# Kernel optimization log

Hardware: AMD Instinct MI355X
Metric: run time of the kernel (lower is better)

The kernel has to match this reference:

```python
import jax, jax.numpy as jnp
import numpy as np

B, S, D = 4, 2048, 1024  # batch, seq_len, d_emb (even for Givens pairs)


def givens_rotate(r, x):
    """Apply 2x2 Givens block rotations defined by r [D] to x [..., D]."""
    g = r.reshape(-1, 2)
    g = g / jnp.linalg.norm(g, axis=-1, keepdims=True)  # normalize (cos, sin) pairs
    xp = x.reshape(x.shape[:-1] + (x.shape[-1] // 2, 2))
    c, s = g[:, 0], g[:, 1]
    y0 = c * xp[..., 0] - s * xp[..., 1]
    y1 = c * xp[..., 1] + s * xp[..., 0]
    return jnp.stack([y0, y1], axis=-1).reshape(x.shape)


def setup_inputs() -> dict:
    key = jax.random.key(0)
    k1, k2 = jax.random.split(key, 2)
    Q = jax.random.normal(k1, (B, S, D), dtype=jnp.float32)
    # QKV_rotation.weight ~ U(-1, 1) per original init (before the identity overwrite)
    rot_w = jax.random.uniform(k2, (3, D), dtype=jnp.float32, minval=-1.0, maxval=1.0)
    scale = jnp.array([np.sqrt(D)], dtype=jnp.float32)
    bias = jnp.zeros((), dtype=jnp.float32)
    return {"Q": Q, "rot_w": rot_w, "scale": scale, "bias": bias}


def reference(Q, rot_w, scale, bias):
    # Givens-rotation 'projections' for q/k/v
    q = givens_rotate(rot_w[0], Q)
    k = givens_rotate(rot_w[1], Q)
    v = givens_rotate(rot_w[2], Q)
    # prepend zero time coordinate -> points on the Lorentz model ambient space
    zeros = jnp.zeros(Q.shape[:-1] + (1,), Q.dtype)
    q = jnp.concatenate([zeros, q], axis=-1)[:, None]  # [B,1,S,D+1]
    k = jnp.concatenate([zeros, k], axis=-1)[:, None]
    v = jnp.concatenate([zeros, v], axis=-1)[:, None]
    # Lorentz signature (-, +, +, ...)
    sgn = jnp.concatenate([-jnp.ones((1,), Q.dtype), jnp.ones((q.shape[-1] - 1,), Q.dtype)])
    # cinner(q, k): time-negated inner product -> scores [B,1,S,S]
    cin = jnp.einsum('bhqd,bhkd->bhqk', q * sgn, k)
    attn = jax.nn.softmax((2.0 + 2.0 * cin) / scale + bias, axis=-1)
    # Lorentz mid-point: weighted sum normalized by sqrt(|<m,m>_L|)
    ave = jnp.einsum('bhqk,bhkd->bhqd', attn, v)
    inner = jnp.sum(ave * ave * sgn, axis=-1, keepdims=True)
    denom = jnp.sqrt(jnp.clip(jnp.abs(inner), 1e-8, None))
    out = (ave / denom)[:, 0]  # [B,S,D+1]
    return out[..., 1:]  # drop time coordinate -> [B,S,D]
```

## Files before the change

### kernel.cpp

```cpp
#include <hip/hip_runtime.h>

typedef _Float16 h16;
typedef _Float16 half8 __attribute__((ext_vector_type(8)));
typedef _Float16 half4v __attribute__((ext_vector_type(4)));
typedef float floatx4 __attribute__((ext_vector_type(4)));

static constexpr int Bb_ = 4, S_ = 2048, D_ = 1024;

static __device__ __forceinline__ void gl_lds16(const void* g, void* l) {
  __builtin_amdgcn_global_load_lds(
      (const __attribute__((address_space(1))) unsigned int*)g,
      (__attribute__((address_space(3))) unsigned int*)l, 16, 0, 0);
}

__global__ __launch_bounds__(256) void k_prep_t(const float* __restrict__ Q,
                                                const float* __restrict__ rot,
                                                h16* __restrict__ Qh,
                                                h16* __restrict__ Kh,
                                                h16* __restrict__ VhT) {
  __shared__ __align__(16) h16 tile[64][64];
  int d0 = blockIdx.x * 64, s0 = blockIdx.y * 64, b = blockIdx.z;
  int t = threadIdx.x;
  const float* Qb = Q + ((size_t)b * S_ + s0) * D_ + d0;
  h16* Qhb = Qh + ((size_t)b * S_ + s0) * D_ + d0;
  h16* Khb = Kh + ((size_t)b * S_ + s0) * D_ + d0;
#pragma unroll
  for (int i = 0; i < 4; ++i) {
    int c = t + 256 * i;
    int row = c >> 4;
    int col = (c & 15) * 4;
    float4 q = *(const float4*)&Qb[(size_t)row * D_ + col];
    int dg = (d0 + col) >> 2;
    float4 r0 = ((const float4*)rot)[dg];
    float4 r1 = ((const float4*)rot)[D_ / 4 + dg];
    float4 r2 = ((const float4*)rot)[2 * D_ / 4 + dg];
    float inq0 = rsqrtf(r0.x * r0.x + r0.y * r0.y);
    float ink0 = rsqrtf(r1.x * r1.x + r1.y * r1.y);
    float cc0 = (r0.x * r1.x + r0.y * r1.y) * inq0 * ink0;
    float ss0 = (r0.x * r1.y - r0.y * r1.x) * inq0 * ink0;
    float y0 = cc0 * q.x - ss0 * q.y;
    float y1 = cc0 * q.y + ss0 * q.x;
    float inq1 = rsqrtf(r0.z * r0.z + r0.w * r0.w);
    float ink1 = rsqrtf(r1.z * r1.z + r1.w * r1.w);
    float cc1 = (r0.z * r1.z + r0.w * r1.w) * inq1 * ink1;
    float ss1 = (r0.z * r1.w - r0.w * r1.z) * inq1 * ink1;
    float y2 = cc1 * q.z - ss1 * q.w;
    float y3 = cc1 * q.w + ss1 * q.z;
    float inv0 = rsqrtf(r2.x * r2.x + r2.y * r2.y);
    float cv0 = r2.x * inv0, sv0 = r2.y * inv0;
    float v0 = cv0 * q.x - sv0 * q.y;
    float v1 = cv0 * q.y + sv0 * q.x;
    float inv1 = rsqrtf(r2.z * r2.z + r2.w * r2.w);
    float cv1 = r2.z * inv1, sv1 = r2.w * inv1;
    float v2 = cv1 * q.z - sv1 * q.w;
    float v3 = cv1 * q.w + sv1 * q.z;
    half4v kh = {(h16)y0, (h16)y1, (h16)y2, (h16)y3};
    half4v qh = {(h16)q.x, (h16)q.y, (h16)q.z, (h16)q.w};
    half4v vh = {(h16)v0, (h16)v1, (h16)v2, (h16)v3};
    *(half4v*)&Qhb[(size_t)row * D_ + col] = qh;
    *(half4v*)&Khb[(size_t)row * D_ + col] = kh;
    int pcol = col ^ ((row >> 3) << 3);
    *(half4v*)&tile[row][pcol] = vh;
  }
  __syncthreads();
  h16* dst = VhT + ((size_t)b * D_ + d0) * S_ + s0;
#pragma unroll
  for (int i = 0; i < 2; ++i) {
    int c = t + 256 * i;
    int drow = c >> 3;
    int sc = (c & 7) * 8;
    int xr = sc;
    half8 v;
#pragma unroll
    for (int j = 0; j < 8; ++j) v[j] = tile[sc + j][drow ^ xr];
    *(half8*)&dst[(size_t)drow * S_ + sc] = v;
  }
}

template <bool OUT16>
__global__ __launch_bounds__(256) void k_gemm_bt(
    const char* __restrict__ A, int a_pitch, unsigned long long a_batch,
    const char* __restrict__ Bt, int b_pitch, unsigned long long b_batch,
    void* __restrict__ C, int c_pitch, unsigned long long c_batch, int Kdim) {
  __shared__ __align__(16) h16 As[2][128 * 32];
  __shared__ __align__(16) h16 Bs[2][128 * 32];
  const int t = threadIdx.x;
  const int lane = t & 63;
  const int w = t >> 6;
  const int wm = (w >> 1) * 64;
  const int wn = (w & 1) * 64;

  const int id = blockIdx.x + gridDim.x * (blockIdx.y + 16 * blockIdx.z);
  const int xcd = id & 7;
  const int s = id >> 3;
  int tm, tn, tz;
  if constexpr (OUT16) {
    tz = s >> 5;
    int tt = s & 31;
    tm = (xcd >> 1) * 4 + (tt >> 3);
    tn = (xcd & 1) * 8 + (tt & 7);
  } else {
    tz = s >> 4;
    int tt = s & 15;
    tm = (xcd >> 1) * 4 + (tt >> 2);
    tn = (xcd & 1) * 4 + (tt & 3);
  }

  const char* Ab = A + (unsigned long long)tz * a_batch +
                   (unsigned long long)tm * 128ull * (unsigned long long)a_pitch;
  const char* Bbp = Bt + (unsigned long long)tz * b_batch +
                    (unsigned long long)tn * 128ull * (unsigned long long)b_pitch;
  const int o0 = t * 16;
  const int o1 = o0 + 4096;
  const int ar0 = o0 >> 6, ar1 = o1 >> 6;
  const int ac0 = ((((o0 >> 4) & 3) ^ ((ar0 >> 1) & 3)) << 4);
  const int ac1 = ((((o1 >> 4) & 3) ^ ((ar1 >> 1) & 3)) << 4);
  const int mrow = lane & 15;
  const int kc = lane >> 4;
  const int koff = ((kc ^ ((mrow >> 1) & 3)) << 3);

  floatx4 acc[4][4];
#pragma unroll
  for (int i = 0; i < 4; ++i)
#pragma unroll
    for (int j = 0; j < 4; ++j) acc[i][j] = (floatx4){0.f, 0.f, 0.f, 0.f};

  for (int kt = 0; kt < Kdim; kt += 64) {
    const int kb = kt * 2;
#pragma unroll
    for (int h = 0; h < 2; ++h) {
      const int hb = kb + h * 64;
      gl_lds16(Ab + (unsigned long long)ar0 * a_pitch + hb + ac0, (char*)As[h] + o0);
      gl_lds16(Ab + (unsigned long long)ar1 * a_pitch + hb + ac1, (char*)As[h] + o1);
      gl_lds16(Bbp + (unsigned long long)ar0 * b_pitch + hb + ac0, (char*)Bs[h] + o0);
      gl_lds16(Bbp + (unsigned long long)ar1 * b_pitch + hb + ac1, (char*)Bs[h] + o1);
    }
    __syncthreads();
#pragma unroll
    for (int h = 0; h < 2; ++h) {
      half8 a[4], b[4];
#pragma unroll
      for (int i = 0; i < 4; ++i)
        a[i] = *(const half8*)&As[h][(wm + i * 16 + mrow) * 32 + koff];
#pragma unroll
      for (int i = 0; i < 4; ++i)
        b[i] = *(const half8*)&Bs[h][(wn + i * 16 + mrow) * 32 + koff];
#pragma unroll
      for (int i = 0; i < 4; ++i)
#pragma unroll
        for (int j = 0; j < 4; ++j)
          acc[i][j] = __builtin_amdgcn_mfma_f32_16x16x32_f16(a[i], b[j], acc[i][j], 0, 0, 0);
    }
    __syncthreads();
  }

  const int m0 = tm * 128 + wm;
  const int n0 = tn * 128 + wn;
  const int col = lane & 15;
  const int rquad = (lane >> 4) * 4;
  if constexpr (OUT16) {
    h16* Cb = (h16*)C + (unsigned long long)tz * c_batch;
#pragma unroll
    for (int i = 0; i < 4; ++i)
#pragma unroll
      for (int j = 0; j < 4; ++j)
#pragma unroll
        for (int r = 0; r < 4; ++r)
          Cb[(unsigned long long)(m0 + i * 16 + rquad + r) * c_pitch + (n0 + j * 16 + col)] =
              (h16)acc[i][j][r];
  } else {
    float* Cb = (float*)C + (unsigned long long)tz * c_batch;
#pragma unroll
    for (int i = 0; i < 4; ++i)
#pragma unroll
      for (int j = 0; j < 4; ++j)
#pragma unroll
        for (int r = 0; r < 4; ++r)
          Cb[(unsigned long long)(m0 + i * 16 + rquad + r) * c_pitch + (n0 + j * 16 + col)] =
              acc[i][j][r];
  }
}

__global__ __launch_bounds__(256) void k_softmax(h16* __restrict__ Sl,
                                                 const float* __restrict__ scale_p) {
  int wv = threadIdx.x >> 6, ln = threadIdx.x & 63;
  int row = blockIdx.x * 4 + wv;
  h16* base = Sl + (size_t)row * S_;
  half8 c[4];
#pragma unroll
  for (int r = 0; r < 4; ++r) c[r] = ((const half8*)base)[ln + 64 * r];
  float m = -1e30f;
#pragma unroll
  for (int r = 0; r < 4; ++r)
#pragma unroll
    for (int j = 0; j < 8; ++j) m = fmaxf(m, (float)c[r][j]);
#pragma unroll
  for (int off = 32; off; off >>= 1) m = fmaxf(m, __shfl_xor(m, off));
  float alpha = 2.0f / scale_p[0];
#pragma unroll
  for (int r = 0; r < 4; ++r) {
    half8 pv;
#pragma unroll
    for (int j = 0; j < 8; ++j) pv[j] = (h16)__expf(((float)c[r][j] - m) * alpha);
    ((half8*)base)[ln + 64 * r] = pv;
  }
}

__global__ __launch_bounds__(256) void k_epilogue(float* __restrict__ O) {
  int wv = threadIdx.x >> 6, ln = threadIdx.x & 63;
  int row = blockIdx.x * 4 + wv;
  float* base = O + (size_t)row * D_;
  float4 u[4];
#pragma unroll
  for (int r = 0; r < 4; ++r) u[r] = ((const float4*)base)[ln + 64 * r];
  float ss = 0.f;
#pragma unroll
  for (int r = 0; r < 4; ++r)
    ss += u[r].x * u[r].x + u[r].y * u[r].y + u[r].z * u[r].z + u[r].w * u[r].w;
#pragma unroll
  for (int off = 32; off; off >>= 1) ss += __shfl_xor(ss, off);
  float f = rsqrtf(fmaxf(ss, 1e-30f));
#pragma unroll
  for (int r = 0; r < 4; ++r) {
    float4 o;
    o.x = u[r].x * f;
    o.y = u[r].y * f;
    o.z = u[r].z * f;
    o.w = u[r].w * f;
    ((float4*)base)[ln + 64 * r] = o;
  }
}

extern "C" void kernel_launch(void* const* d_in, const int* in_sizes, int n_in,
                              void* d_out, int out_size, void* d_ws, size_t ws_size,
                              hipStream_t stream) {
  const float* Q = (const float*)d_in[0];
  const float* rot = (const float*)d_in[1];
  const float* scale = (const float*)d_in[2];
  float* O = (float*)d_out;
  char* ws = (char*)d_ws;
  const size_t MB = 1024ull * 1024ull;
  h16* Qh = (h16*)(ws);
  h16* Kh = (h16*)(ws + 16 * MB);
  h16* VhT = (h16*)(ws + 32 * MB);
  h16* Sl = (h16*)(ws + 48 * MB);

  k_prep_t<<<dim3(D_ / 64, S_ / 64, Bb_), 256, 0, stream>>>(Q, rot, Qh, Kh, VhT);
  k_gemm_bt<true><<<dim3(S_ / 128, S_ / 128, Bb_), 256, 0, stream>>>(
      (const char*)Qh, D_ * 2, (unsigned long long)S_ * D_ * 2,
      (const char*)Kh, D_ * 2, (unsigned long long)S_ * D_ * 2,
      (void*)Sl, S_, (unsigned long long)S_ * S_, D_);
  k_softmax<<<dim3(Bb_ * S_ / 4), 256, 0, stream>>>(Sl, scale);
  k_gemm_bt<false><<<dim3(D_ / 128, S_ / 128, Bb_), 256, 0, stream>>>(
      (const char*)Sl, S_ * 2, (unsigned long long)S_ * S_ * 2,
      (const char*)VhT, S_ * 2, (unsigned long long)D_ * S_ * 2,
      (void*)O, D_, (unsigned long long)S_ * D_, S_);
  k_epilogue<<<dim3(Bb_ * S_ / 4), 256, 0, stream>>>(O);
}
```

Before: 209.2 us.

## Replace 128x128 GEMM with 8-wave 256-row tiled, prefetch-pipelined GEMM

Replaces the 4-wave 128x128 tile GEMM with an 8-wave, 512-thread kernel using 256x256 (QK^T) or 256x128 (PV) tiles. It double-buffers LDS, issues global-to-LDS loads for future k-tiles between MFMA quads, and uses explicit vmcnt waits, barriers and s_setprio to overlap loads with compute. Block-to-tile mapping is changed to group tiles per XCD. The larger per-thread accumulator footprint may lower occupancy, and the fine-grained barrier schedule is fragile.

```diff
diff --git a/kernel.cpp b/kernel.cpp
--- a/kernel.cpp
+++ b/kernel.cpp
@@ -77,108 +77,185 @@
   }
 }
 
-template <bool OUT16>
-__global__ __launch_bounds__(256) void k_gemm_bt(
+#define G_FENCE asm volatile("" ::: "memory")
+#define G_BAR                     \
+  do {                            \
+    G_FENCE;                      \
+    __builtin_amdgcn_s_barrier(); \
+    G_FENCE;                      \
+  } while (0)
+
+template <int NF, bool OUT16>
+__global__ __launch_bounds__(512) void k_gemm8(
     const char* __restrict__ A, int a_pitch, unsigned long long a_batch,
     const char* __restrict__ Bt, int b_pitch, unsigned long long b_batch,
     void* __restrict__ C, int c_pitch, unsigned long long c_batch, int Kdim) {
-  __shared__ __align__(16) h16 As[2][128 * 32];
-  __shared__ __align__(16) h16 Bs[2][128 * 32];
+  constexpr int BNR = NF * 64;
+  constexpr int JQ = NF / 2;
+  __shared__ __align__(16) h16 As[2][2][256 * 32];
+  __shared__ __align__(16) h16 Bs[2][2][BNR * 32];
   const int t = threadIdx.x;
   const int lane = t & 63;
   const int w = t >> 6;
-  const int wm = (w >> 1) * 64;
-  const int wn = (w & 1) * 64;
-
-  const int id = blockIdx.x + gridDim.x * (blockIdx.y + 16 * blockIdx.z);
-  const int xcd = id & 7;
-  const int s = id >> 3;
-  int tm, tn, tz;
-  if constexpr (OUT16) {
-    tz = s >> 5;
-    int tt = s & 31;
-    tm = (xcd >> 1) * 4 + (tt >> 3);
-    tn = (xcd & 1) * 8 + (tt & 7);
-  } else {
-    tz = s >> 4;
-    int tt = s & 15;
-    tm = (xcd >> 1) * 4 + (tt >> 2);
-    tn = (xcd & 1) * 4 + (tt & 3);
-  }
-
+  const int wm = (w >> 2) * 128;
+  const int wn = (w & 3) * (NF * 16);
+  const int id = blockIdx.x + 8 * (blockIdx.y + 8 * blockIdx.z);
+  const int L = (id & 7) * 32 + (id >> 3);
+  const int tm = L & 7, tn = (L >> 3) & 7, tz = L >> 6;
   const char* Ab = A + (unsigned long long)tz * a_batch +
-                   (unsigned long long)tm * 128ull * (unsigned long long)a_pitch;
-  const char* Bbp = Bt + (unsigned long long)tz * b_batch +
-                    (unsigned long long)tn * 128ull * (unsigned long long)b_pitch;
-  const int o0 = t * 16;
-  const int o1 = o0 + 4096;
-  const int ar0 = o0 >> 6, ar1 = o1 >> 6;
-  const int ac0 = ((((o0 >> 4) & 3) ^ ((ar0 >> 1) & 3)) << 4);
-  const int ac1 = ((((o1 >> 4) & 3) ^ ((ar1 >> 1) & 3)) << 4);
-  const int mrow = lane & 15;
-  const int kc = lane >> 4;
-  const int koff = ((kc ^ ((mrow >> 1) & 3)) << 3);
-
-  floatx4 acc[4][4];
-#pragma unroll
-  for (int i = 0; i < 4; ++i)
-#pragma unroll
-    for (int j = 0; j < 4; ++j) acc[i][j] = (floatx4){0.f, 0.f, 0.f, 0.f};
-
-  for (int kt = 0; kt < Kdim; kt += 64) {
-    const int kb = kt * 2;
-#pragma unroll
-    for (int h = 0; h < 2; ++h) {
-      const int hb = kb + h * 64;
-      gl_lds16(Ab + (unsigned long long)ar0 * a_pitch + hb + ac0, (char*)As[h] + o0);
-      gl_lds16(Ab + (unsigned long long)ar1 * a_pitch + hb + ac1, (char*)As[h] + o1);
-      gl_lds16(Bbp + (unsigned long long)ar0 * b_pitch + hb + ac0, (char*)Bs[h] + o0);
-      gl_lds16(Bbp + (unsigned long long)ar1 * b_pitch + hb + ac1, (char*)Bs[h] + o1);
-    }
-    __syncthreads();
-#pragma unroll
-    for (int h = 0; h < 2; ++h) {
-      half8 a[4], b[4];
-#pragma unroll
-      for (int i = 0; i < 4; ++i)
-        a[i] = *(const half8*)&As[h][(wm + i * 16 + mrow) * 32 + koff];
-#pragma unroll
-      for (int i = 0; i < 4; ++i)
-        b[i] = *(const half8*)&Bs[h][(wn + i * 16 + mrow) * 32 + koff];
-#pragma unroll
-      for (int i = 0; i < 4; ++i)
-#pragma unroll
-        for (int j = 0; j < 4; ++j)
-          acc[i][j] = __builtin_amdgcn_mfma_f32_16x16x32_f16(a[i], b[j], acc[i][j], 0, 0, 0);
-    }
-    __syncthreads();
-  }
-
-  const int m0 = tm * 128 + wm;
-  const int n0 = tn * 128 + wn;
-  const int col = lane & 15;
-  const int rquad = (lane >> 4) * 4;
+                   (unsigned long long)(tm * 256) * (unsigned long long)a_pitch;
+  const char* Bb = Bt + (unsigned long long)tz * b_batch +
+                   (unsigned long long)(tn * BNR) * (unsigned long long)b_pitch;
+  const int srow = t >> 2;
+  const int scol = ((t & 3) ^ ((t >> 3) & 3)) << 4;
+  const int lds_o = t * 16;
+  const int mrow = lane & 15, kc = lane >> 4;
+  const int koff = (kc ^ ((mrow >> 1) & 3)) << 3;
+  const int NT = Kdim >> 6;
+
+#define SG_A(bf, kt, hm)                                                      \
+  do {                                                                        \
+    const char* sp_ = Ab +                                                    \
+                      (unsigned long long)(srow + (hm) * 128) * a_pitch +     \
+                      (kt) * 128 + scol;                                      \
+    gl_lds16(sp_, (char*)&As[bf][0][(hm) * 128 * 32] + lds_o);                \
+    gl_lds16(sp_ + 64, (char*)&As[bf][1][(hm) * 128 * 32] + lds_o);           \
+  } while (0)
+#define SG_B(bf, kt, hm)                                                      \
+  do {                                                                        \
+    const char* sp_ = Bb +                                                    \
+                      (unsigned long long)(srow + (hm) * 128) * b_pitch +     \
+                      (kt) * 128 + scol;                                      \
+    gl_lds16(sp_, (char*)&Bs[bf][0][(hm) * 128 * 32] + lds_o);                \
+    gl_lds16(sp_ + 64, (char*)&Bs[bf][1][(hm) * 128 * 32] + lds_o);           \
+  } while (0)
+
+  half8 a[4][2], b[2][JQ][2];
+  floatx4 acc[8][NF];
+#pragma unroll
+  for (int i = 0; i < 8; ++i)
+#pragma unroll
+    for (int j = 0; j < NF; ++j) acc[i][j] = (floatx4){0.f, 0.f, 0.f, 0.f};
+
+#define LDA_(bf, mh)                                                           \
+  do {                                                                         \
+    _Pragma("unroll") for (int i_ = 0; i_ < 4; ++i_) {                         \
+      a[i_][0] = *(const half8*)&As[bf][0]                                     \
+                     [(wm + ((mh) * 4 + i_) * 16 + mrow) * 32 + koff];         \
+      a[i_][1] = *(const half8*)&As[bf][1]                                     \
+                     [(wm + ((mh) * 4 + i_) * 16 + mrow) * 32 + koff];         \
+    }                                                                          \
+  } while (0)
+#define LDB_(bf, nh)                                                           \
+  do {                                                                         \
+    _Pragma("unroll") for (int j_ = 0; j_ < JQ; ++j_) {                        \
+      b[nh][j_][0] = *(const half8*)&Bs[bf][0]                                 \
+                         [(wn + ((nh) * JQ + j_) * 16 + mrow) * 32 + koff];    \
+      b[nh][j_][1] = *(const half8*)&Bs[bf][1]                                 \
+                         [(wn + ((nh) * JQ + j_) * 16 + mrow) * 32 + koff];    \
+    }                                                                          \
+  } while (0)
+#define QUAD(mh, nh)                                                           \
+  do {                                                                         \
+    __builtin_amdgcn_s_setprio(1);                                             \
+    _Pragma("unroll") for (int i_ = 0; i_ < 4; ++i_)                           \
+        _Pragma("unroll") for (int j_ = 0; j_ < JQ; ++j_) {                    \
+      acc[(mh) * 4 + i_][(nh) * JQ + j_] =                                     \
+          __builtin_amdgcn_mfma_f32_16x16x32_f16(                              \
+              a[i_][0], b[nh][j_][0], acc[(mh) * 4 + i_][(nh) * JQ + j_], 0,   \
+              0, 0);                                                           \
+      acc[(mh) * 4 + i_][(nh) * JQ + j_] =                                     \
+          __builtin_amdgcn_mfma_f32_16x16x32_f16(                              \
+              a[i_][1], b[nh][j_][1], acc[(mh) * 4 + i_][(nh) * JQ + j_], 0,   \
+              0, 0);                                                           \
+    }                                                                          \
+    __builtin_amdgcn_s_setprio(0);                                             \
+  } while (0)
+
+  SG_A(0, 0, 0);
+  SG_A(0, 0, 1);
+  SG_B(0, 0, 0);
+  if constexpr (NF == 4) SG_B(0, 0, 1);
+  SG_B(1, 1, 0);
+  if constexpr (NF == 4) SG_B(1, 1, 1);
+  SG_A(1, 1, 0);
+  if constexpr (NF == 4)
+    asm volatile("s_waitcnt vmcnt(6)" ::: "memory");
+  else
+    asm volatile("s_waitcnt vmcnt(4)" ::: "memory");
+  G_BAR;
+
+#define TILE_(bf, nb, u)                                                       \
+  do {                                                                         \
+    const int k1_ = ((u) + 1 < NT) ? (u) + 1 : NT - 1;                         \
+    const int k2_ = ((u) + 2 < NT) ? (u) + 2 : NT - 1;                         \
+                                                                       \
+    LDA_(bf, 0);                                                               \
+    LDB_(bf, 0);                                                               \
+    SG_A(nb, k1_, 1);                                                          \
+    G_BAR;                                                                     \
+    QUAD(0, 0);                                                                \
+    G_BAR;                                                                     \
+                                                                       \
+    LDB_(bf, 1);                                                               \
+    G_BAR;                                                                     \
+    QUAD(0, 1);                                                                \
+    G_BAR;                                                                     \
+                                                                       \
+    LDA_(bf, 1);                                                               \
+    SG_B(bf, k2_, 0);                                                          \
+    G_BAR;                                                                     \
+    QUAD(1, 0);                                                                \
+    G_BAR;                                                                     \
+                                                                       \
+    if constexpr (NF == 4) SG_B(bf, k2_, 1);                                   \
+    SG_A(bf, k2_, 0);                                                          \
+    if constexpr (NF == 4)                                                     \
+      asm volatile("s_waitcnt vmcnt(6)" ::: "memory");                         \
+    else                                                                       \
+      asm volatile("s_waitcnt vmcnt(4)" ::: "memory");                         \
+    G_BAR;                                                                     \
+    QUAD(1, 1);                                                                \
+    G_BAR;                                                                     \
+  } while (0)
+
+  for (int u = 0; u < NT; u += 2) {
+    TILE_(0, 1, u);
+    TILE_(1, 0, u + 1);
+  }
+  asm volatile("s_waitcnt vmcnt(0)" ::: "memory");
+
+  const int m0 = tm * 256 + wm;
+  const int n0 = tn * BNR + wn;
+  const int ccol = lane & 15;
+  const int rq = (lane >> 4) * 4;
   if constexpr (OUT16) {
     h16* Cb = (h16*)C + (unsigned long long)tz * c_batch;
 #pragma unroll
-    for (int i = 0; i < 4; ++i)
-#pragma unroll
-      for (int j = 0; j < 4; ++j)
+    for (int i = 0; i < 8; ++i)
+#pragma unroll
+      for (int j = 0; j < NF; ++j)
 #pragma unroll
         for (int r = 0; r < 4; ++r)
-          Cb[(unsigned long long)(m0 + i * 16 + rquad + r) * c_pitch + (n0 + j * 16 + col)] =
-              (h16)acc[i][j][r];
+          Cb[(unsigned long long)(m0 + i * 16 + rq + r) * c_pitch +
+             (n0 + j * 16 + ccol)] = (h16)acc[i][j][r];
   } else {
     float* Cb = (float*)C + (unsigned long long)tz * c_batch;
 #pragma unroll
-    for (int i = 0; i < 4; ++i)
-#pragma unroll
-      for (int j = 0; j < 4; ++j)
+    for (int i = 0; i < 8; ++i)
+#pragma unroll
+      for (int j = 0; j < NF; ++j)
 #pragma unroll
         for (int r = 0; r < 4; ++r)
-          Cb[(unsigned long long)(m0 + i * 16 + rquad + r) * c_pitch + (n0 + j * 16 + col)] =
-              acc[i][j][r];
-  }
+          Cb[(unsigned long long)(m0 + i * 16 + rq + r) * c_pitch +
+             (n0 + j * 16 + ccol)] = acc[i][j][r];
+  }
+#undef TILE_
+#undef QUAD
+#undef LDB_
+#undef LDA_
+#undef SG_B
+#undef SG_A
 }
 
 __global__ __launch_bounds__(256) void k_softmax(h16* __restrict__ Sl,
@@ -246,12 +323,12 @@
   h16* Sl = (h16*)(ws + 48 * MB);
 
   k_prep_t<<<dim3(D_ / 64, S_ / 64, Bb_), 256, 0, stream>>>(Q, rot, Qh, Kh, VhT);
-  k_gemm_bt<true><<<dim3(S_ / 128, S_ / 128, Bb_), 256, 0, stream>>>(
+  k_gemm8<4, true><<<dim3(8, 8, 4), 512, 0, stream>>>(
       (const char*)Qh, D_ * 2, (unsigned long long)S_ * D_ * 2,
       (const char*)Kh, D_ * 2, (unsigned long long)S_ * D_ * 2,
       (void*)Sl, S_, (unsigned long long)S_ * S_, D_);
   k_softmax<<<dim3(Bb_ * S_ / 4), 256, 0, stream>>>(Sl, scale);
-  k_gemm_bt<false><<<dim3(D_ / 128, S_ / 128, Bb_), 256, 0, stream>>>(
+  k_gemm8<2, false><<<dim3(8, 8, 4), 512, 0, stream>>>(
       (const char*)Sl, S_ * 2, (unsigned long long)S_ * S_ * 2,
       (const char*)VhT, S_ * 2, (unsigned long long)D_ * S_ * 2,
       (void*)O, D_, (unsigned long long)S_ * D_, S_);
```

After: 194.2 us. -7.1%, faster.
